# Kernel optimization log

Hardware: AMD Instinct MI355X
Metric: run time of the kernel (lower is better)

The kernel has to match this reference:

```python
import jax, jax.numpy as jnp
import numpy as np


def setup_inputs() -> dict:
    key = jax.random.key(0)
    k1, k2, k3 = jax.random.split(key, 3)
    B, T, D = 2, 2048, 1024
    x = jax.random.normal(k1, (B, T, D), dtype=jnp.float32)
    w_qkv = jax.random.normal(k2, (3 * D, D), dtype=jnp.float32) * (D ** -0.5)
    w_out = jax.random.normal(k3, (D, D), dtype=jnp.float32) * (D ** -0.5)
    return {"x": x, "w_qkv": w_qkv, "w_out": w_out, "heads": 16}


def reference(x, w_qkv, w_out, heads):
    # SelfAttention forward: attention_type='sdp', position_mode='alibi', causal=True, eval mode.
    B, T, D = x.shape
    H = heads
    hd = D // H
    scale = hd ** -0.5

    # qkv projection: torch Linear -> x @ W^T
    qkv = (x @ w_qkv.T).reshape(B, T, 3, H, hd)
    qkv = jnp.transpose(qkv, (2, 0, 3, 1, 4))  # [3, B, H, T, hd]
    q, k, v = qkv[0], qkv[1], qkv[2]

    # ALiBi relative bias: slopes = 1 / 2^(h/H) for h = 1..H
    slopes = 1.0 / jnp.power(2.0, jnp.arange(1, H + 1, dtype=jnp.float32) / H)
    pos = jnp.arange(T, dtype=jnp.float32)
    rel = jnp.abs(pos[:, None] - pos[None, :])  # [T, T]
    bias = -slopes[None, :, None, None] * rel[None, None, :, :]  # [1, H, T, T]

    # scores + causal mask + softmax (manual path since position_bias is not None)
    scores = jnp.einsum('bhqd,bhkd->bhqk', q, k) * scale + bias
    causal_mask = jnp.triu(jnp.ones((T, T), dtype=bool), k=1)
    scores = jnp.where(causal_mask[None, None, :, :], -jnp.inf, scores)
    attn = jax.nn.softmax(scores, axis=-1)
    attn = jnp.where(jnp.isnan(attn), 1.0 / float(max(T, 1)), attn)

    out = jnp.einsum('bhqk,bhkd->bhqd', attn, v)  # [B, H, T, hd]
    out = jnp.transpose(out, (0, 2, 1, 3)).reshape(B, T, D)
    return out @ w_out.T
```

## Files before the change

### kernel.cpp

```cpp
#include <hip/hip_runtime.h>
#include <hip/hip_bf16.h>

typedef __attribute__((ext_vector_type(8))) short shortx8;
typedef __attribute__((ext_vector_type(4))) float floatx4;
typedef __attribute__((ext_vector_type(4))) unsigned uintx4;
typedef __attribute__((ext_vector_type(2))) unsigned uintx2;

#define B_ 2
#define T_ 2048
#define D_ 1024
#define H_ 16
#define HD_ 64
#define SCALE 0.125f
#define SMAX 16.0f
#define FULLH ((size_t)B_ * H_ * T_ * HD_)

#define GLDS16(g, l) __builtin_amdgcn_global_load_lds( \
    (__attribute__((address_space(1))) void*)(g), \
    (__attribute__((address_space(3))) void*)(l), 16, 0, 0)

__device__ __forceinline__ short f2bf(float f) {
    union { float f; unsigned u; } v; v.f = f;
    unsigned r = v.u + 0x7FFFu + ((v.u >> 16) & 1u);
    return (short)(r >> 16);
}

__device__ __forceinline__ unsigned pk2(float x, float y) {
    union { __hip_bfloat162 h; unsigned u; } t;
    t.h = __float22bfloat162_rn(make_float2(x, y));
    return t.u;
}

__device__ __forceinline__ shortx8 cvt8(floatx4 a, floatx4 b) {
    uintx4 r = { pk2(a[0], a[1]), pk2(a[2], a[3]), pk2(b[0], b[1]), pk2(b[2], b[3]) };
    return __builtin_bit_cast(shortx8, r);
}

__global__ __launch_bounds__(256) void cvt_bf(const float* __restrict__ src,
                                              short* __restrict__ dst, int n8) {
    int i = blockIdx.x * 256 + threadIdx.x;
    if (i < n8) {
        const floatx4* p = reinterpret_cast<const floatx4*>(src) + (size_t)i * 2;
        *(reinterpret_cast<shortx8*>(dst) + i) = cvt8(p[0], p[1]);
    }
}


__global__ __launch_bounds__(256) void qkv_fast(const short* __restrict__ xbf,
                                                const short* __restrict__ wbf,
                                                short* __restrict__ qout,
                                                short* __restrict__ kv) {
    __shared__ __align__(16) short As[128 * 64];
    __shared__ __align__(16) short Bs[128 * 64];

    const int tid = threadIdx.x;
    const int wv = tid >> 6;
    const int l  = tid & 63;
    const int ln = l & 15;
    const int quad = l >> 4;
    const int rowb = quad << 2;
    const int wm = wv >> 1, wn = wv & 1;
    const int m0 = blockIdx.y * 128;
    const int n0g = blockIdx.x * 128;

    const int lr = l >> 3, lc = l & 7;
    const int gcol = (lc ^ lr) << 3;
    const short* agp = xbf + (size_t)(m0 + wv * 32 + lr) * D_ + gcol;
    const short* bgp = wbf + (size_t)(n0g + wv * 32 + lr) * D_ + gcol;
    short* aldsb = As + wv * 32 * 64;
    short* bldsb = Bs + wv * 32 * 64;

    floatx4 acc[4][4] = {};

    for (int k0 = 0; k0 < D_; k0 += 64) {
        __syncthreads();
#pragma unroll
        for (int c = 0; c < 4; ++c) {
            GLDS16(agp + (size_t)(c * 8) * D_ + k0, aldsb + c * 512);
            GLDS16(bgp + (size_t)(c * 8) * D_ + k0, bldsb + c * 512);
        }
        __syncthreads();

#pragma unroll
        for (int kk = 0; kk < 2; ++kk) {
            const int csw = (kk << 2) + quad;
            const int sw = (csw ^ (ln & 7)) << 3;
            shortx8 af[4], bf[4];
#pragma unroll
            for (int i = 0; i < 4; ++i)
                af[i] = *reinterpret_cast<const shortx8*>(&As[((wm * 64 + i * 16 + ln) << 6) + sw]);
#pragma unroll
            for (int j = 0; j < 4; ++j)
                bf[j] = *reinterpret_cast<const shortx8*>(&Bs[((wn * 64 + j * 16 + ln) << 6) + sw]);
#pragma unroll
            for (int i = 0; i < 4; ++i)
#pragma unroll
                for (int j = 0; j < 4; ++j)
                    acc[i][j] = __builtin_amdgcn_mfma_f32_16x16x32_bf16(af[i], bf[j], acc[i][j], 0, 0, 0);
        }
    }

    const int sel = n0g >> 10;
    const int bb = m0 >> 11;
    const int t0w = (m0 + wm * 64) & (T_ - 1);
    const int h = ((n0g + wn * 64) >> 6) & 15;

    if (sel < 2) {
        short* dst = (sel == 0) ? qout : kv;
        const float sc = (sel == 0) ? SCALE : 1.0f;
        const size_t hb = (size_t)(bb * H_ + h) * T_;
#pragma unroll
        for (int i = 0; i < 4; ++i)
#pragma unroll
            for (int r = 0; r < 4; ++r) {
                int t = t0w + i * 16 + rowb + r;
#pragma unroll
                for (int j = 0; j < 4; ++j)
                    dst[(hb + t) * HD_ + j * 16 + ln] = f2bf(acc[i][j][r] * sc);
            }
    } else {
        __syncthreads();
        short* tb = (wv < 2) ? (As + wv * 4096) : (Bs + (wv - 2) * 4096);
        short* vhead = kv + FULLH + (size_t)(bb * H_ + h) * HD_ * T_;
        const int dl = l & 31, th = (l >> 5) << 5;
#pragma unroll
        for (int p = 0; p < 2; ++p) {
#pragma unroll
            for (int i = 0; i < 4; ++i)
#pragma unroll
                for (int jj = 0; jj < 2; ++jj) {
                    int j = 2 * p + jj;
#pragma unroll
                    for (int r = 0; r < 4; ++r)
                        tb[(jj * 16 + ln) * 72 + i * 16 + rowb + r] = f2bf(acc[i][j][r]);
                }
            short* vd = vhead + (size_t)(p * 32 + dl) * T_ + t0w + th;
#pragma unroll
            for (int seg = 0; seg < 4; ++seg)
                *reinterpret_cast<shortx8*>(vd + seg * 8) =
                    *reinterpret_cast<const shortx8*>(&tb[dl * 72 + th + seg * 8]);
        }
    }
}

__global__ __launch_bounds__(256) void out_fast(const short* __restrict__ Abf,
                                                const short* __restrict__ wbf,
                                                float* __restrict__ out) {
    __shared__ __align__(16) short As[128 * 64];
    __shared__ __align__(16) short Bs[128 * 64];

    const int tid = threadIdx.x;
    const int wv = tid >> 6;
    const int l  = tid & 63;
    const int ln = l & 15;
    const int quad = l >> 4;
    const int rowb = quad << 2;
    const int wm = wv >> 1, wn = wv & 1;
    const int m0 = blockIdx.y * 128;
    const int n0g = blockIdx.x * 128;

    const int lr = l >> 3, lc = l & 7;
    const int gcol = (lc ^ lr) << 3;
    const short* bgp = wbf + (size_t)(n0g + wv * 32 + lr) * D_ + gcol;
    short* aldsb = As + wv * 32 * 64;
    short* bldsb = Bs + wv * 32 * 64;

    size_t abase[4];
#pragma unroll
    for (int c = 0; c < 4; ++c) {
        int m = m0 + wv * 32 + c * 8 + lr;
        int bb2 = m >> 11, t = m & (T_ - 1);
        abase[c] = ((size_t)(bb2 * H_) * T_ + t) * HD_ + gcol;
    }

    floatx4 acc[4][4] = {};

    for (int k0 = 0; k0 < D_; k0 += 64) {
        const size_t hoff = (size_t)(k0 >> 6) * T_ * HD_;
        __syncthreads();
#pragma unroll
        for (int c = 0; c < 4; ++c) {
            GLDS16(Abf + abase[c] + hoff, aldsb + c * 512);
            GLDS16(bgp + (size_t)(c * 8) * D_ + k0, bldsb + c * 512);
        }
        __syncthreads();

#pragma unroll
        for (int kk = 0; kk < 2; ++kk) {
            const int csw = (kk << 2) + quad;
            const int sw = (csw ^ (ln & 7)) << 3;
            shortx8 af[4], bf[4];
#pragma unroll
            for (int i = 0; i < 4; ++i)
                af[i] = *reinterpret_cast<const shortx8*>(&As[((wm * 64 + i * 16 + ln) << 6) + sw]);
#pragma unroll
            for (int j = 0; j < 4; ++j)
                bf[j] = *reinterpret_cast<const shortx8*>(&Bs[((wn * 64 + j * 16 + ln) << 6) + sw]);
#pragma unroll
            for (int i = 0; i < 4; ++i)
#pragma unroll
                for (int j = 0; j < 4; ++j)
                    acc[i][j] = __builtin_amdgcn_mfma_f32_16x16x32_bf16(af[i], bf[j], acc[i][j], 0, 0, 0);
        }
    }

#pragma unroll
    for (int i = 0; i < 4; ++i)
#pragma unroll
        for (int r = 0; r < 4; ++r) {
            int m = m0 + wm * 64 + i * 16 + rowb + r;
#pragma unroll
            for (int j = 0; j < 4; ++j)
                out[(size_t)m * D_ + n0g + wn * 64 + j * 16 + ln] = acc[i][j][r];
        }
}

__global__ __launch_bounds__(256, 4) void attn(const short* __restrict__ qws,
                                               const short* __restrict__ kv,
                                               short* ao) {
    __shared__ __align__(16) short Ks[64][72];
    __shared__ __align__(16) short Vt[64][72];
    __shared__ __align__(16) short Pt[4][64][20];

    const int tid = threadIdx.x;
    const int wv   = tid >> 6;
    const int l    = tid & 63;
    const int ln   = l & 15;
    const int quad = l >> 4;
    const int qd   = quad << 3;
    const int rowb = quad << 2;

    const int xcd  = blockIdx.x & 7;
    const int slot = blockIdx.x >> 3;
    const int bh   = xcd * 4 + (slot & 3);
    const int qb   = 31 - (slot >> 2);
    const int h    = bh & 15;
    const int b    = bh >> 4;

    const float slope = exp2f(-(float)(h + 1) * (1.0f / 16.0f));
    const size_t koff = (size_t)(b * H_ + h) * T_ * HD_;
    const int q0 = qb * 64 + wv * 16;

    shortx8 qf[2];
#pragma unroll
    for (int kk = 0; kk < 2; ++kk)
        qf[kk] = *reinterpret_cast<const shortx8*>(&qws[koff + (size_t)(q0 + ln) * HD_ + kk * 32 + qd]);

    const int r0 = tid >> 3, c0 = (tid & 7) << 3, r1 = r0 + 32;
    const short* kbase = kv + koff;
    const short* vbase = kv + FULLH + koff;
    shortx8 kA, kB, vA, vB;
    auto FETCH = [&](int kb) {
        const short* kp = kbase + ((size_t)(kb * 64) << 6);
        kA = *reinterpret_cast<const shortx8*>(kp + ((size_t)r0 << 6) + c0);
        kB = *reinterpret_cast<const shortx8*>(kp + ((size_t)r1 << 6) + c0);
        const short* vp = vbase + kb * 64;
        vA = *reinterpret_cast<const shortx8*>(vp + ((size_t)r0 << 11) + c0);
        vB = *reinterpret_cast<const shortx8*>(vp + ((size_t)r1 << 11) + c0);
    };

    floatx4 oacc[4] = {};
    floatx4 lsum = {};
    const shortx8 ones = {16256, 16256, 16256, 16256, 16256, 16256, 16256, 16256};
    const float base0 = -SMAX - slope * (float)(q0 + rowb);

    FETCH(0);
    for (int kb = 0; kb <= qb; ++kb) {
        __syncthreads();
        *reinterpret_cast<shortx8*>(&Ks[r0][c0]) = kA;
        *reinterpret_cast<shortx8*>(&Ks[r1][c0]) = kB;
        *reinterpret_cast<shortx8*>(&Vt[r0][c0]) = vA;
        *reinterpret_cast<shortx8*>(&Vt[r1][c0]) = vB;
        __syncthreads();
        if (kb < qb) FETCH(kb + 1);

        const bool diag = (kb == qb);
        const int ncmax = diag ? (wv + 1) : 4;
        const int kln = kb * 64 + ln;
        const float bb0 = slope * (float)kln + base0;

#pragma unroll
        for (int nc = 0; nc < 4; ++nc) {
            floatx4 s = {};
            if (nc < ncmax) {
#pragma unroll
                for (int kk = 0; kk < 2; ++kk) {
                    shortx8 bfr = *reinterpret_cast<const shortx8*>(&Ks[nc * 16 + ln][kk * 32 + qd]);
                    s = __builtin_amdgcn_mfma_f32_16x16x32_bf16(qf[kk], bfr, s, 0, 0, 0);
                }
            }
            float p[4];
#pragma unroll
            for (int r = 0; r < 4; ++r) {
                bool ok = (kln + nc * 16) <= (q0 + rowb + r);
                float e = __expf(s[r] + bb0 + slope * (float)(nc * 16 - r));
                p[r] = ok ? e : 0.0f;
            }
            uintx2 pkd = { pk2(p[0], p[1]), pk2(p[2], p[3]) };
            *reinterpret_cast<uintx2*>(&Pt[wv][nc * 16 + ln][rowb]) = pkd;
        }

#pragma unroll
        for (int kk = 0; kk < 2; ++kk) {
            if (diag && kk * 32 > wv * 16 + 15) continue;
            shortx8 pf;
#pragma unroll
            for (int j = 0; j < 8; ++j) pf[j] = Pt[wv][kk * 32 + qd + j][ln];
            lsum = __builtin_amdgcn_mfma_f32_16x16x32_bf16(pf, ones, lsum, 0, 0, 0);
#pragma unroll
            for (int nc = 0; nc < 4; ++nc) {
                shortx8 bfr = *reinterpret_cast<const shortx8*>(&Vt[nc * 16 + ln][kk * 32 + qd]);
                oacc[nc] = __builtin_amdgcn_mfma_f32_16x16x32_bf16(pf, bfr, oacc[nc], 0, 0, 0);
            }
        }
    }

#pragma unroll
    for (int r = 0; r < 4; ++r) {
        float inv = 1.0f / lsum[r];
        int t = q0 + rowb + r;
#pragma unroll
        for (int nc = 0; nc < 4; ++nc)
            ao[koff + (size_t)t * HD_ + nc * 16 + ln] = f2bf(oacc[nc][r] * inv);
    }
}

__global__ __launch_bounds__(256) void qkv_slow(const float* __restrict__ x,
                                                const float* __restrict__ wqkv,
                                                short* __restrict__ qout,
                                                short* __restrict__ kv) {
    __shared__ __align__(16) short As[64][72];
    __shared__ __align__(16) short Bs[64][72];
    const int tid = threadIdx.x;
    const int wv = tid >> 6, l = tid & 63, ln = l & 15, quad = l >> 4, qd = quad << 3;
    const int m0 = blockIdx.y * 64;
    const int sel = blockIdx.x >> 4, h = blockIdx.x & 15;
    const int nrow = sel * D_ + h * HD_;
    const int sr0 = tid >> 3, sc0 = (tid & 7) << 3, sr1 = sr0 + 32;
    floatx4 fa[4], fb[4];
    auto FETCH = [&](int k0) {
        const float* ap = &x[(size_t)(m0 + sr0) * D_ + k0 + sc0];
        fa[0] = *reinterpret_cast<const floatx4*>(ap);
        fa[1] = *reinterpret_cast<const floatx4*>(ap + 4);
        ap += (size_t)32 * D_;
        fa[2] = *reinterpret_cast<const floatx4*>(ap);
        fa[3] = *reinterpret_cast<const floatx4*>(ap + 4);
        const float* bp = &wqkv[(size_t)(nrow + sr0) * D_ + k0 + sc0];
        fb[0] = *reinterpret_cast<const floatx4*>(bp);
        fb[1] = *reinterpret_cast<const floatx4*>(bp + 4);
        bp += (size_t)32 * D_;
        fb[2] = *reinterpret_cast<const floatx4*>(bp);
        fb[3] = *reinterpret_cast<const floatx4*>(bp + 4);
    };
    floatx4 acc[4] = {};
    FETCH(0);
    for (int k0 = 0; k0 < D_; k0 += 64) {
        __syncthreads();
        *reinterpret_cast<shortx8*>(&As[sr0][sc0]) = cvt8(fa[0], fa[1]);
        *reinterpret_cast<shortx8*>(&As[sr1][sc0]) = cvt8(fa[2], fa[3]);
        *reinterpret_cast<shortx8*>(&Bs[sr0][sc0]) = cvt8(fb[0], fb[1]);
        *reinterpret_cast<shortx8*>(&Bs[sr1][sc0]) = cvt8(fb[2], fb[3]);
        __syncthreads();
        if (k0 + 64 < D_) FETCH(k0 + 64);
        const int mr = (wv << 4) + ln;
#pragma unroll
        for (int kk = 0; kk < 2; ++kk) {
            shortx8 a = *reinterpret_cast<const shortx8*>(&As[mr][kk * 32 + qd]);
#pragma unroll
            for (int nc = 0; nc < 4; ++nc) {
                shortx8 b = *reinterpret_cast<const shortx8*>(&Bs[nc * 16 + ln][kk * 32 + qd]);
                acc[nc] = __builtin_amdgcn_mfma_f32_16x16x32_bf16(a, b, acc[nc], 0, 0, 0);
            }
        }
    }
    const int bb = m0 >> 11, t0 = m0 & (T_ - 1);
    if (sel < 2) {
        short* dst = (sel == 0) ? qout : kv;
        const float sc = (sel == 0) ? SCALE : 1.0f;
#pragma unroll
        for (int r = 0; r < 4; ++r) {
            int t = t0 + (wv << 4) + (quad << 2) + r;
#pragma unroll
            for (int nc = 0; nc < 4; ++nc)
                dst[((size_t)(bb * H_ + h) * T_ + t) * HD_ + nc * 16 + ln] = f2bf(acc[nc][r] * sc);
        }
    } else {
        __syncthreads();
#pragma unroll
        for (int r = 0; r < 4; ++r)
#pragma unroll
            for (int nc = 0; nc < 4; ++nc)
                As[nc * 16 + ln][(wv << 4) + (quad << 2) + r] = f2bf(acc[nc][r]);
        __syncthreads();
        const int d = tid >> 2, tseg = (tid & 3) << 4;
        short* vdst = kv + FULLH + ((size_t)(bb * H_ + h) * HD_ + d) * T_ + t0 + tseg;
        *reinterpret_cast<shortx8*>(vdst)     = *reinterpret_cast<const shortx8*>(&As[d][tseg]);
        *reinterpret_cast<shortx8*>(vdst + 8) = *reinterpret_cast<const shortx8*>(&As[d][tseg + 8]);
    }
}

__global__ __launch_bounds__(256) void out_slow(const short* __restrict__ A,
                                                const float* __restrict__ W,
                                                float* __restrict__ out) {
    __shared__ __align__(16) short As[64][72];
    __shared__ __align__(16) short Bs[64][72];
    const int tid = threadIdx.x;
    const int wv = tid >> 6, l = tid & 63, ln = l & 15, quad = l >> 4, qd = quad << 3;
    const int m0 = blockIdx.y * 64, n0 = blockIdx.x * 64;
    const int sr0 = tid >> 3, sc0 = (tid & 7) << 3, sr1 = sr0 + 32;
    shortx8 sa0, sa1;
    floatx4 fb[4];
    auto FETCH = [&](int k0) {
        const int h = k0 >> 6;
        int m = m0 + sr0;
        int bb = m >> 11, t = m & (T_ - 1);
        sa0 = *reinterpret_cast<const shortx8*>(A + ((size_t)(bb * H_ + h) * T_ + t) * HD_ + sc0);
        m = m0 + sr1; bb = m >> 11; t = m & (T_ - 1);
        sa1 = *reinterpret_cast<const shortx8*>(A + ((size_t)(bb * H_ + h) * T_ + t) * HD_ + sc0);
        const float* bp = &W[(size_t)(n0 + sr0) * D_ + k0 + sc0];
        fb[0] = *reinterpret_cast<const floatx4*>(bp);
        fb[1] = *reinterpret_cast<const floatx4*>(bp + 4);
        bp += (size_t)32 * D_;
        fb[2] = *reinterpret_cast<const floatx4*>(bp);
        fb[3] = *reinterpret_cast<const floatx4*>(bp + 4);
    };
    floatx4 acc[4] = {};
    FETCH(0);
    for (int k0 = 0; k0 < D_; k0 += 64) {
        __syncthreads();
        *reinterpret_cast<shortx8*>(&As[sr0][sc0]) = sa0;
        *reinterpret_cast<shortx8*>(&As[sr1][sc0]) = sa1;
        *reinterpret_cast<shortx8*>(&Bs[sr0][sc0]) = cvt8(fb[0], fb[1]);
        *reinterpret_cast<shortx8*>(&Bs[sr1][sc0]) = cvt8(fb[2], fb[3]);
        __syncthreads();
        if (k0 + 64 < D_) FETCH(k0 + 64);
        const int mr = (wv << 4) + ln;
#pragma unroll
        for (int kk = 0; kk < 2; ++kk) {
            shortx8 a = *reinterpret_cast<const shortx8*>(&As[mr][kk * 32 + qd]);
#pragma unroll
            for (int nc = 0; nc < 4; ++nc) {
                shortx8 b = *reinterpret_cast<const shortx8*>(&Bs[nc * 16 + ln][kk * 32 + qd]);
                acc[nc] = __builtin_amdgcn_mfma_f32_16x16x32_bf16(a, b, acc[nc], 0, 0, 0);
            }
        }
    }
#pragma unroll
    for (int r = 0; r < 4; ++r) {
        int m = m0 + (wv << 4) + (quad << 2) + r;
#pragma unroll
        for (int nc = 0; nc < 4; ++nc)
            out[(size_t)m * D_ + n0 + nc * 16 + ln] = acc[nc][r];
    }
}

extern "C" void kernel_launch(void* const* d_in, const int* in_sizes, int n_in,
                              void* d_out, int out_size, void* d_ws, size_t ws_size,
                              hipStream_t stream) {
    const float* x    = (const float*)d_in[0];
    const float* wqkv = (const float*)d_in[1];
    const float* wout = (const float*)d_in[2];

    short* kvbuf = (short*)d_out;
    float* out   = (float*)d_out;

    if (ws_size >= 23068672ULL) {
        short* xbf  = (short*)d_ws;
        short* wbf  = xbf + 4 * 1024 * 1024;
        short* qws  = xbf + 7 * 1024 * 1024;
        short* wobf = xbf;

        cvt_bf<<<2048, 256, 0, stream>>>(x, xbf, 524288);
        cvt_bf<<<1536, 256, 0, stream>>>(wqkv, wbf, 393216);
        qkv_fast<<<dim3(24, 32), 256, 0, stream>>>(xbf, wbf, qws, kvbuf);
        cvt_bf<<<512, 256, 0, stream>>>(wout, wobf, 131072);
        attn<<<dim3(1024), 256, 0, stream>>>(qws, kvbuf, qws);
        out_fast<<<dim3(8, 32), 256, 0, stream>>>(qws, wobf, out);
    } else {
        short* qws = (short*)d_ws;
        qkv_slow<<<dim3(48, 64), 256, 0, stream>>>(x, wqkv, qws, kvbuf);
        attn<<<dim3(1024), 256, 0, stream>>>(qws, kvbuf, qws);
        out_slow<<<dim3(16, 64), 256, 0, stream>>>(qws, wout, out);
    }
}
```

Before: 192.1 us.

## Pair causal query tiles per attention block; fuse input casts and fold Q scale

Each attention block now processes two query tiles, slot and 31-slot. It streams K/V once across both tiles, so every block gets the same amount of causal work and the K/V loads are shared. The grid drops to 512 blocks and the launch-bounds occupancy hint drops from 4 to 2 to make room for the doubled accumulators. The x and w_qkv bf16 conversions are merged into one launch, and the attention scale is folded into the Q rows of the weight during conversion instead of the GEMM epilogue. The trade-off is higher register pressure and fewer resident waves per CU in exchange for balanced work and less K/V traffic.

```diff
diff --git a/kernel.cpp b/kernel.cpp
--- a/kernel.cpp
+++ b/kernel.cpp
@@ -36,6 +36,23 @@
     return __builtin_bit_cast(shortx8, r);
 }
 
+__global__ __launch_bounds__(256) void cvt_xw(const float* __restrict__ x,
+                                              const float* __restrict__ w,
+                                              short* __restrict__ xbf,
+                                              short* __restrict__ wbf) {
+    int i = blockIdx.x * 256 + threadIdx.x;
+    if (i < 524288) {
+        const floatx4* p = reinterpret_cast<const floatx4*>(x) + (size_t)i * 2;
+        *(reinterpret_cast<shortx8*>(xbf) + i) = cvt8(p[0], p[1]);
+    } else {
+        int j = i - 524288;
+        const floatx4* p = reinterpret_cast<const floatx4*>(w) + (size_t)j * 2;
+        floatx4 a = p[0], b = p[1];
+        if (j < 131072) { a *= SCALE; b *= SCALE; }
+        *(reinterpret_cast<shortx8*>(wbf) + j) = cvt8(a, b);
+    }
+}
+
 __global__ __launch_bounds__(256) void cvt_bf(const float* __restrict__ src,
                                               short* __restrict__ dst, int n8) {
     int i = blockIdx.x * 256 + threadIdx.x;
@@ -44,7 +61,6 @@
         *(reinterpret_cast<shortx8*>(dst) + i) = cvt8(p[0], p[1]);
     }
 }
-
 
 __global__ __launch_bounds__(256) void qkv_fast(const short* __restrict__ xbf,
                                                 const short* __restrict__ wbf,
@@ -107,7 +123,6 @@
 
     if (sel < 2) {
         short* dst = (sel == 0) ? qout : kv;
-        const float sc = (sel == 0) ? SCALE : 1.0f;
         const size_t hb = (size_t)(bb * H_ + h) * T_;
 #pragma unroll
         for (int i = 0; i < 4; ++i)
@@ -116,7 +131,7 @@
                 int t = t0w + i * 16 + rowb + r;
 #pragma unroll
                 for (int j = 0; j < 4; ++j)
-                    dst[(hb + t) * HD_ + j * 16 + ln] = f2bf(acc[i][j][r] * sc);
+                    dst[(hb + t) * HD_ + j * 16 + ln] = f2bf(acc[i][j][r]);
             }
     } else {
         __syncthreads();
@@ -215,7 +230,7 @@
         }
 }
 
-__global__ __launch_bounds__(256, 4) void attn(const short* __restrict__ qws,
+__global__ __launch_bounds__(256, 2) void attn(const short* __restrict__ qws,
                                                const short* __restrict__ kv,
                                                short* ao) {
     __shared__ __align__(16) short Ks[64][72];
@@ -231,20 +246,27 @@
     const int rowb = quad << 2;
 
     const int xcd  = blockIdx.x & 7;
-    const int slot = blockIdx.x >> 3;
-    const int bh   = xcd * 4 + (slot & 3);
-    const int qb   = 31 - (slot >> 2);
+    const int idx  = blockIdx.x >> 3;
+    const int bh   = xcd * 4 + (idx & 3);
+    const int slot = idx >> 2;
     const int h    = bh & 15;
     const int b    = bh >> 4;
 
     const float slope = exp2f(-(float)(h + 1) * (1.0f / 16.0f));
     const size_t koff = (size_t)(b * H_ + h) * T_ * HD_;
-    const int q0 = qb * 64 + wv * 16;
-
-    shortx8 qf[2];
-#pragma unroll
-    for (int kk = 0; kk < 2; ++kk)
-        qf[kk] = *reinterpret_cast<const shortx8*>(&qws[koff + (size_t)(q0 + ln) * HD_ + kk * 32 + qd]);
+
+    const int qbt[2] = { slot, 31 - slot };
+    int q0[2]; float base0[2];
+    shortx8 qf[2][2];
+#pragma unroll
+    for (int qt = 0; qt < 2; ++qt) {
+        q0[qt] = qbt[qt] * 64 + wv * 16;
+        base0[qt] = -SMAX - slope * (float)(q0[qt] + rowb);
+#pragma unroll
+        for (int kk = 0; kk < 2; ++kk)
+            qf[qt][kk] = *reinterpret_cast<const shortx8*>(
+                &qws[koff + (size_t)(q0[qt] + ln) * HD_ + kk * 32 + qd]);
+    }
 
     const int r0 = tid >> 3, c0 = (tid & 7) << 3, r1 = r0 + 32;
     const short* kbase = kv + koff;
@@ -259,70 +281,77 @@
         vB = *reinterpret_cast<const shortx8*>(vp + ((size_t)r1 << 11) + c0);
     };
 
-    floatx4 oacc[4] = {};
-    floatx4 lsum = {};
+    floatx4 oacc[2][4] = {};
+    floatx4 lsum[2] = {};
     const shortx8 ones = {16256, 16256, 16256, 16256, 16256, 16256, 16256, 16256};
-    const float base0 = -SMAX - slope * (float)(q0 + rowb);
+    const int kbmax = qbt[1];
 
     FETCH(0);
-    for (int kb = 0; kb <= qb; ++kb) {
+    for (int kb = 0; kb <= kbmax; ++kb) {
         __syncthreads();
         *reinterpret_cast<shortx8*>(&Ks[r0][c0]) = kA;
         *reinterpret_cast<shortx8*>(&Ks[r1][c0]) = kB;
         *reinterpret_cast<shortx8*>(&Vt[r0][c0]) = vA;
         *reinterpret_cast<shortx8*>(&Vt[r1][c0]) = vB;
         __syncthreads();
-        if (kb < qb) FETCH(kb + 1);
-
-        const bool diag = (kb == qb);
-        const int ncmax = diag ? (wv + 1) : 4;
+        if (kb < kbmax) FETCH(kb + 1);
+
         const int kln = kb * 64 + ln;
-        const float bb0 = slope * (float)kln + base0;
-
-#pragma unroll
-        for (int nc = 0; nc < 4; ++nc) {
-            floatx4 s = {};
-            if (nc < ncmax) {
-#pragma unroll
-                for (int kk = 0; kk < 2; ++kk) {
-                    shortx8 bfr = *reinterpret_cast<const shortx8*>(&Ks[nc * 16 + ln][kk * 32 + qd]);
-                    s = __builtin_amdgcn_mfma_f32_16x16x32_bf16(qf[kk], bfr, s, 0, 0, 0);
+
+#pragma unroll
+        for (int qt = 0; qt < 2; ++qt) {
+            if (kb > qbt[qt]) continue;
+            const bool diag = (kb == qbt[qt]);
+            const int ncmax = diag ? (wv + 1) : 4;
+            const float bb0 = slope * (float)kln + base0[qt];
+
+#pragma unroll
+            for (int nc = 0; nc < 4; ++nc) {
+                floatx4 s = {};
+                if (nc < ncmax) {
+#pragma unroll
+                    for (int kk = 0; kk < 2; ++kk) {
+                        shortx8 bfr = *reinterpret_cast<const shortx8*>(&Ks[nc * 16 + ln][kk * 32 + qd]);
+                        s = __builtin_amdgcn_mfma_f32_16x16x32_bf16(qf[qt][kk], bfr, s, 0, 0, 0);
+                    }
+                }
+                float p[4];
+#pragma unroll
+                for (int r = 0; r < 4; ++r) {
+                    bool ok = (kln + nc * 16) <= (q0[qt] + rowb + r);
+                    float e = __expf(s[r] + bb0 + slope * (float)(nc * 16 - r));
+                    p[r] = ok ? e : 0.0f;
+                }
+                uintx2 pkd = { pk2(p[0], p[1]), pk2(p[2], p[3]) };
+                *reinterpret_cast<uintx2*>(&Pt[wv][nc * 16 + ln][rowb]) = pkd;
+            }
+
+#pragma unroll
+            for (int kk = 0; kk < 2; ++kk) {
+                if (diag && kk * 32 > wv * 16 + 15) continue;
+                shortx8 pf;
+#pragma unroll
+                for (int j = 0; j < 8; ++j) pf[j] = Pt[wv][kk * 32 + qd + j][ln];
+                lsum[qt] = __builtin_amdgcn_mfma_f32_16x16x32_bf16(pf, ones, lsum[qt], 0, 0, 0);
+#pragma unroll
+                for (int nc = 0; nc < 4; ++nc) {
+                    shortx8 bfr = *reinterpret_cast<const shortx8*>(&Vt[nc * 16 + ln][kk * 32 + qd]);
+                    oacc[qt][nc] = __builtin_amdgcn_mfma_f32_16x16x32_bf16(pf, bfr, oacc[qt][nc], 0, 0, 0);
                 }
             }
-            float p[4];
-#pragma unroll
-            for (int r = 0; r < 4; ++r) {
-                bool ok = (kln + nc * 16) <= (q0 + rowb + r);
-                float e = __expf(s[r] + bb0 + slope * (float)(nc * 16 - r));
-                p[r] = ok ? e : 0.0f;
-            }
-            uintx2 pkd = { pk2(p[0], p[1]), pk2(p[2], p[3]) };
-            *reinterpret_cast<uintx2*>(&Pt[wv][nc * 16 + ln][rowb]) = pkd;
-        }
-
-#pragma unroll
-        for (int kk = 0; kk < 2; ++kk) {
-            if (diag && kk * 32 > wv * 16 + 15) continue;
-            shortx8 pf;
-#pragma unroll
-            for (int j = 0; j < 8; ++j) pf[j] = Pt[wv][kk * 32 + qd + j][ln];
-            lsum = __builtin_amdgcn_mfma_f32_16x16x32_bf16(pf, ones, lsum, 0, 0, 0);
-#pragma unroll
-            for (int nc = 0; nc < 4; ++nc) {
-                shortx8 bfr = *reinterpret_cast<const shortx8*>(&Vt[nc * 16 + ln][kk * 32 + qd]);
-                oacc[nc] = __builtin_amdgcn_mfma_f32_16x16x32_bf16(pf, bfr, oacc[nc], 0, 0, 0);
-            }
-        }
-    }
-
-#pragma unroll
-    for (int r = 0; r < 4; ++r) {
-        float inv = 1.0f / lsum[r];
-        int t = q0 + rowb + r;
-#pragma unroll
-        for (int nc = 0; nc < 4; ++nc)
-            ao[koff + (size_t)t * HD_ + nc * 16 + ln] = f2bf(oacc[nc][r] * inv);
-    }
+        }
+    }
+
+#pragma unroll
+    for (int qt = 0; qt < 2; ++qt)
+#pragma unroll
+        for (int r = 0; r < 4; ++r) {
+            float inv = 1.0f / lsum[qt][r];
+            int t = q0[qt] + rowb + r;
+#pragma unroll
+            for (int nc = 0; nc < 4; ++nc)
+                ao[koff + (size_t)t * HD_ + nc * 16 + ln] = f2bf(oacc[qt][nc][r] * inv);
+        }
 }
 
 __global__ __launch_bounds__(256) void qkv_slow(const float* __restrict__ x,
@@ -470,16 +499,15 @@
         short* qws  = xbf + 7 * 1024 * 1024;
         short* wobf = xbf;
 
-        cvt_bf<<<2048, 256, 0, stream>>>(x, xbf, 524288);
-        cvt_bf<<<1536, 256, 0, stream>>>(wqkv, wbf, 393216);
+        cvt_xw<<<3584, 256, 0, stream>>>(x, wqkv, xbf, wbf);
         qkv_fast<<<dim3(24, 32), 256, 0, stream>>>(xbf, wbf, qws, kvbuf);
         cvt_bf<<<512, 256, 0, stream>>>(wout, wobf, 131072);
-        attn<<<dim3(1024), 256, 0, stream>>>(qws, kvbuf, qws);
+        attn<<<dim3(512), 256, 0, stream>>>(qws, kvbuf, qws);
         out_fast<<<dim3(8, 32), 256, 0, stream>>>(qws, wobf, out);
     } else {
         short* qws = (short*)d_ws;
         qkv_slow<<<dim3(48, 64), 256, 0, stream>>>(x, wqkv, qws, kvbuf);
-        attn<<<dim3(1024), 256, 0, stream>>>(qws, kvbuf, qws);
+        attn<<<dim3(512), 256, 0, stream>>>(qws, kvbuf, qws);
         out_slow<<<dim3(16, 64), 256, 0, stream>>>(qws, wout, out);
     }
 }
```

After: 208.3 us. 1.08x slower.
